# Kernel optimization log

Measured on AMD Instinct MI355X. Metric: run time of the kernel, lower is better.

The kernel has to match this reference:

```python
import jax, jax.numpy as jnp
import numpy as np

N_NODES = 100000
N_EDGES = 1200000
NODE_IN = 64
EDGE_IN = 32
HIDDEN = 64


def _glorot(key, shape):
    fan_in, fan_out = shape[0], shape[1]
    s = jnp.sqrt(2.0 / (fan_in + fan_out))
    return jax.random.normal(key, shape, dtype=jnp.float32) * s


def setup_inputs() -> dict:
    key = jax.random.key(0)
    ks = jax.random.split(key, 16)
    inp = {
        "x": jax.random.normal(ks[0], (N_NODES, NODE_IN), dtype=jnp.float32),
        "edge_index": jax.random.randint(ks[1], (2, N_EDGES), 0, N_NODES, dtype=jnp.int64),
        "edge_attr": jax.random.normal(ks[2], (N_EDGES, EDGE_IN), dtype=jnp.float32),
        # SAGE layer 0 (in=NODE_IN -> HIDDEN): lin_l (neighbors, has bias), lin_r (root)
        "w_l0": _glorot(ks[3], (NODE_IN, HIDDEN)),
        "w_r0": _glorot(ks[4], (NODE_IN, HIDDEN)),
        "b0": jnp.zeros((HIDDEN,), jnp.float32),
        "ln_g0": jnp.ones((HIDDEN,), jnp.float32),
        "ln_b0": jnp.zeros((HIDDEN,), jnp.float32),
        # SAGE layer 1 (HIDDEN -> HIDDEN)
        "w_l1": _glorot(ks[5], (HIDDEN, HIDDEN)),
        "w_r1": _glorot(ks[6], (HIDDEN, HIDDEN)),
        "b1": jnp.zeros((HIDDEN,), jnp.float32),
        "ln_g1": jnp.ones((HIDDEN,), jnp.float32),
        "ln_b1": jnp.zeros((HIDDEN,), jnp.float32),
        # Edge classifier MLP: in_dim = 3*HIDDEN + EDGE_IN = 224
        "cw1": _glorot(ks[7], (3 * HIDDEN + EDGE_IN, HIDDEN)),
        "cb1": jnp.zeros((HIDDEN,), jnp.float32),
        "cw2": _glorot(ks[8], (HIDDEN, HIDDEN // 2)),
        "cb2": jnp.zeros((HIDDEN // 2,), jnp.float32),
        "cw3": _glorot(ks[9], (HIDDEN // 2, 1)),
        "cb3": jnp.zeros((1,), jnp.float32),
    }
    return inp


def _sage_conv(x, src, dst, w_l, w_r, b):
    # mean-aggregate source features at destination nodes (PyG SAGEConv, aggr='mean')
    n = x.shape[0]
    msg = x[src]  # [E, F] gather
    agg = jax.ops.segment_sum(msg, dst, num_segments=n)
    cnt = jax.ops.segment_sum(jnp.ones((src.shape[0], 1), x.dtype), dst, num_segments=n)
    mean = agg / jnp.maximum(cnt, 1.0)
    return mean @ w_l + x @ w_r + b


def _layer_norm(x, g, b, eps=1e-5):
    mu = jnp.mean(x, axis=-1, keepdims=True)
    var = jnp.var(x, axis=-1, keepdims=True)
    return (x - mu) * jax.lax.rsqrt(var + eps) * g + b


def reference(x, edge_index, edge_attr,
              w_l0, w_r0, b0, ln_g0, ln_b0,
              w_l1, w_r1, b1, ln_g1, ln_b1,
              cw1, cb1, cw2, cb2, cw3, cb3):
    src, dst = edge_index[0], edge_index[1]
    # Encoder (eval mode: dropout is identity)
    h = jax.nn.relu(_layer_norm(_sage_conv(x, src, dst, w_l0, w_r0, b0), ln_g0, ln_b0))
    z = jax.nn.relu(_layer_norm(_sage_conv(h, src, dst, w_l1, w_r1, b1), ln_g1, ln_b1))
    # Edge classifier: gather-concat-MLP
    z_src = z[src]
    z_dst = z[dst]
    edge_repr = jnp.concatenate([z_src, z_dst, z_src * z_dst, edge_attr], axis=-1)
    h1 = jax.nn.relu(edge_repr @ cw1 + cb1)
    h2 = jax.nn.relu(h1 @ cw2 + cb2)
    logits = (h2 @ cw3 + cb3).squeeze(-1)  # [E]
    return logits
```

## Files before the change

kernel.cpp:

```cpp
#include <hip/hip_runtime.h>
#include <hip/hip_bf16.h>

#define N_NODES 100000
#define N_EDGES 1200000

typedef __attribute__((ext_vector_type(8))) short bfrag;
typedef __attribute__((ext_vector_type(4))) float ffrag;
typedef __attribute__((ext_vector_type(4))) float nf4;
typedef __attribute__((ext_vector_type(2))) float nf2;

union FragU { uint4 v; uint32_t u[4]; bfrag f; };

__device__ __forceinline__ ushort bfbits(float a) {
  union { __hip_bfloat16 h; ushort u; } c; c.h = __float2bfloat16(a); return c.u;
}
__device__ __forceinline__ uint32_t pkbf(float a, float b) {
  union { __hip_bfloat162 h; uint32_t u; } c;
  c.h = __float22bfloat162_rn(float2{a, b}); return c.u;
}
__device__ __forceinline__ uint32_t mul2bf(uint32_t a, uint32_t b) {
  union { uint32_t u; __hip_bfloat162 h; } x, y, r;
  x.u = a; y.u = b; r.h = __hmul2(x.h, y.h); return r.u;
}
__device__ __forceinline__ float bflo(uint32_t u) { return __int_as_float(u << 16); }
__device__ __forceinline__ float bfhi(uint32_t u) { return __int_as_float(u & 0xffff0000u); }

template <int CTRL>
__device__ __forceinline__ float dpp_add16(float v) {
  int x = __builtin_amdgcn_update_dpp(0, __float_as_int(v), CTRL, 0xF, 0xF, true);
  return v + __int_as_float(x);
}
__device__ __forceinline__ float reduce16(float v) {
  v = dpp_add16<0xB1>(v);
  v = dpp_add16<0x4E>(v);
  v = dpp_add16<0x141>(v);
  v = dpp_add16<0x140>(v);
  return v;
}


__global__ void cvt_k(const float* __restrict__ x, ushort* __restrict__ xb, int n2) {
  int i = blockIdx.x * blockDim.x + threadIdx.x;
  if (i < n2) {
    nf2 v = __builtin_nontemporal_load(((const nf2*)x) + i);
    ((uint32_t*)xb)[i] = pkbf(v.x, v.y);
  }
}


__global__ void hist_k(const int* __restrict__ ei, int* __restrict__ deg,
                       int* __restrict__ rank, int E) {
  int e = blockIdx.x * blockDim.x + threadIdx.x;
  if (e < E) rank[e] = atomicAdd(&deg[ei[E + e]], 1);
}

__global__ __launch_bounds__(1024) void scan1_k(const int* __restrict__ deg,
                                                int* __restrict__ off,
                                                int* __restrict__ bsum, int n) {
  __shared__ int wpart[16];
  __shared__ int wpre[16];
  int tid = threadIdx.x, lane = tid & 63, wid = tid >> 6;
  int i = blockIdx.x * 1024 + tid;
  int v = (i < n) ? deg[i] : 0;
  int x = v;
  #pragma unroll
  for (int o = 1; o < 64; o <<= 1) {
    int y = __shfl_up(x, o);
    if (lane >= o) x += y;
  }
  if (lane == 63) wpart[wid] = x;
  __syncthreads();
  if (tid == 0) {
    int run = 0;
    #pragma unroll
    for (int w = 0; w < 16; w++) { int t = wpart[w]; wpre[w] = run; run += t; }
    bsum[blockIdx.x] = run;
  }
  __syncthreads();
  if (i < n) off[i] = x - v + wpre[wid];
}

__global__ void scan2_k(const int* __restrict__ bsum, int* __restrict__ bpre,
                        int* __restrict__ off, int nb, int n) {
  if (threadIdx.x == 0) {
    int run = 0;
    for (int b = 0; b < nb; b++) { int t = bsum[b]; bpre[b] = run; run += t; }
    off[n] = run;
  }
}

__global__ __launch_bounds__(1024) void scan3_k(int* __restrict__ off,
                                                const int* __restrict__ bpre, int n) {
  int i = blockIdx.x * 1024 + threadIdx.x;
  if (i < n) off[i] += bpre[blockIdx.x];
}

__global__ void fill_k(const int* __restrict__ ei, const int* __restrict__ off,
                       const int* __restrict__ rank, int* __restrict__ csr, int E) {
  int e = blockIdx.x * blockDim.x + threadIdx.x;
  if (e < E) {
    int d = ei[E + e];
    int p = off[d] + rank[e];
    __builtin_nontemporal_store(ei[e], &csr[p]);
  }
}


__global__ __launch_bounds__(256) void agg_k(
    const ushort* __restrict__ Xb, const int* __restrict__ off, const int* __restrict__ csr,
    ushort* __restrict__ aggout, int n) {
  int lane = threadIdx.x & 63;
  int quad = lane >> 4, f8 = lane & 15;
  int wave = blockIdx.x * 4 + (threadIdx.x >> 6);
  int nw = gridDim.x * 4;
  int nquads = (n + 3) >> 2;
  const uint2* X2 = (const uint2*)Xb;
  for (int p = wave; p < nquads; p += nw) {
    int i = p * 4 + quad;
    int ic = i < n ? i : n - 1;
    int s0 = off[ic], s1 = off[ic + 1];
    float a0 = 0.f, a1 = 0.f, a2 = 0.f, a3 = 0.f;
    for (int j = s0; j < s1; j += 16) {
      int id[16]; uint2 us[16];
      #pragma unroll
      for (int u = 0; u < 16; u++) {
        int jj = j + u;
        id[u] = csr[jj < s1 ? jj : s1 - 1];
      }
      #pragma unroll
      for (int u = 0; u < 16; u++) us[u] = X2[(size_t)id[u] * 16 + f8];
      #pragma unroll
      for (int u = 0; u < 16; u++) {
        if (j + u < s1) {
          a0 += bflo(us[u].x); a1 += bfhi(us[u].x);
          a2 += bflo(us[u].y); a3 += bfhi(us[u].y);
        }
      }
    }
    if (i < n) {
      float rdeg = 1.f / fmaxf((float)(s1 - s0), 1.f);
      uint2 w;
      w.x = pkbf(a0 * rdeg, a1 * rdeg);
      w.y = pkbf(a2 * rdeg, a3 * rdeg);
      ((uint2*)aggout)[(size_t)i * 16 + f8] = w;
    }
  }
}


__global__ __launch_bounds__(256) void node_k(
    const ushort* __restrict__ agg, const ushort* __restrict__ selfb,
    const float* __restrict__ wl, const float* __restrict__ wr,
    const float* __restrict__ bias, const float* __restrict__ g, const float* __restrict__ lb,
    ushort* __restrict__ outb, int n) {
  __shared__ ushort wt[64 * 128];
  const int tid = threadIdx.x;
  for (int i = tid; i < 8192; i += 256) {
    int k = i >> 6, nn = i & 63;
    float v = (k < 64) ? wl[k * 64 + nn] : wr[(k - 64) * 64 + nn];
    wt[nn * 128 + (((k >> 3) ^ (nn & 7)) * 8) + (k & 7)] = bfbits(v);
  }
  __syncthreads();
  const int lane = tid & 63, wid = tid >> 6;
  const int ln = lane & 15, q = lane >> 4;
  float bias_n[4], g_n[4], lb_n[4];
  #pragma unroll
  for (int nt = 0; nt < 4; nt++) {
    bias_n[nt] = bias[nt * 16 + ln];
    g_n[nt] = g[nt * 16 + ln];
    lb_n[nt] = lb[nt * 16 + ln];
  }
  const int ntiles = (n + 15) >> 4;
  const int S = gridDim.x * 4;
  int t0 = blockIdx.x * 4 + wid;

  auto loadfrag = [&](FragU (&afr)[4], int t) {
    int tc = t < ntiles ? t : ntiles - 1;
    int node = tc * 16 + ln;
    int nc = node < n ? node : n - 1;
    #pragma unroll
    for (int kk = 0; kk < 2; kk++) {
      afr[kk].v     = ((const uint4*)agg)[(size_t)nc * 8 + kk * 4 + q];
      afr[2 + kk].v = ((const uint4*)selfb)[(size_t)nc * 8 + kk * 4 + q];
    }
  };

  auto compute = [&](FragU (&afr)[4], int t) {
    ffrag acc[4];
    #pragma unroll
    for (int nt = 0; nt < 4; nt++) acc[nt] = ffrag{0.f, 0.f, 0.f, 0.f};
    #pragma unroll
    for (int kk = 0; kk < 4; kk++) {
      bfrag a = afr[kk].f;
      #pragma unroll
      for (int nt = 0; nt < 4; nt++) {
        int nn = nt * 16 + ln;
        int b = kk * 4 + q;
        const bfrag* bp = (const bfrag*)&wt[nn * 128 + ((b ^ (nn & 7)) * 8)];
        acc[nt] = __builtin_amdgcn_mfma_f32_16x16x32_bf16(a, *bp, acc[nt], 0, 0, 0);
      }
    }
    #pragma unroll
    for (int r = 0; r < 4; r++) {
      int m = t * 16 + q * 4 + r;
      float o[4];
      #pragma unroll
      for (int nt = 0; nt < 4; nt++) o[nt] = acc[nt][r] + bias_n[nt];
      float s = (o[0] + o[1]) + (o[2] + o[3]);
      s = reduce16(s);
      float mu = s * (1.f / 64.f);
      float v2 = 0.f;
      #pragma unroll
      for (int nt = 0; nt < 4; nt++) { float d2 = o[nt] - mu; v2 += d2 * d2; }
      v2 = reduce16(v2);
      float rs = rsqrtf(v2 * (1.f / 64.f) + 1e-5f);
      if (m < n) {
        #pragma unroll
        for (int nt = 0; nt < 4; nt++) {
          float y = fmaxf((o[nt] - mu) * rs * g_n[nt] + lb_n[nt], 0.f);
          outb[(size_t)m * 64 + nt * 16 + ln] = bfbits(y);
        }
      }
    }
  };

  if (t0 >= ntiles) return;
  FragU fA[4], fB[4];
  loadfrag(fA, t0);
  loadfrag(fB, t0 + S);
  for (int t = t0; t < ntiles; t += 2 * S) {
    compute(fA, t);
    loadfrag(fA, t + 2 * S);
    if (t + S < ntiles) compute(fB, t + S);
    loadfrag(fB, t + 3 * S);
  }
}


__global__ __launch_bounds__(256, 2) void edge_mfma_k(
    const int* __restrict__ ei, const float* __restrict__ ea,
    const ushort* __restrict__ zb,
    const float* __restrict__ cw1, const float* __restrict__ cb1,
    const float* __restrict__ cw2, const float* __restrict__ cb2,
    const float* __restrict__ cw3, const float* __restrict__ cb3,
    float* __restrict__ out, int E) {
  __shared__ ushort smem[64 * 256];
  __shared__ ushort ws2[2048];
  const int tid = threadIdx.x;

  for (int i = tid; i < 224 * 64; i += 256) {
    int k = i >> 6, n = i & 63;
    int blk = k >> 3;
    smem[n * 256 + ((blk ^ (n & 7)) * 8) + (k & 7)] = bfbits(cw1[i]);
  }
  __syncthreads();

  const int lane = tid & 63, wid = tid >> 6;
  const int ln = lane & 15, q = lane >> 4;

  FragU w1f[7][4];
  #pragma unroll
  for (int kk = 0; kk < 7; kk++) {
    #pragma unroll
    for (int tt = 0; tt < 4; tt++) {
      int n = tt * 16 + ln;
      int b = kk * 4 + q;
      w1f[kk][tt].v = *(const uint4*)&smem[n * 256 + ((b ^ (n & 7)) * 8)];
    }
  }
  if (wid == 0) {
    #pragma unroll
    for (int t2 = 0; t2 < 2; t2++) {
      #pragma unroll
      for (int kk = 0; kk < 2; kk++) {
        uint32_t w[4];
        #pragma unroll
        for (int p = 0; p < 4; p++) {
          int k = kk * 32 + q * 8 + p * 2;
          int n = t2 * 16 + ln;
          w[p] = pkbf(cw2[k * 32 + n], cw2[(k + 1) * 32 + n]);
        }
        *(uint4*)&ws2[((t2 * 2 + kk) * 64 + lane) * 8] = make_uint4(w[0], w[1], w[2], w[3]);
      }
    }
  }
  __syncthreads();
  ushort* hb = &smem[wid * 1024];

  float cb1v[4];
  #pragma unroll
  for (int t = 0; t < 4; t++) cb1v[t] = cb1[t * 16 + ln];
  float cb2a = cb2[ln], cb2b = cb2[16 + ln];
  float w3a = cw3[ln], w3b = cw3[16 + ln];
  float cb3v = cb3[0];

  const int nt = E >> 4;
  const int S = gridDim.x * 4;
  const int S3 = 3 * S;
  const int w0 = blockIdx.x * 4 + wid;
  const uint4* Z4 = (const uint4*)zb;
  const nf4* EA4 = (const nf4*)ea;

  FragU zA[4], zB[4], zC[4];
  int svA, dvA, svB, dvB, svC, dvC;

  auto prol = [&](FragU (&z)[4], int &sv, int &dv, int u) {
    int uc = u < nt ? u : nt - 1;
    int e = uc * 16 + ln;
    int s = __builtin_nontemporal_load(ei + e);
    int d = __builtin_nontemporal_load(ei + E + e);
    z[0].v = Z4[(size_t)s * 8 + q];
    z[1].v = Z4[(size_t)s * 8 + 4 + q];
    z[2].v = Z4[(size_t)d * 8 + q];
    z[3].v = Z4[(size_t)d * 8 + 4 + q];
    int un = u + S3 < nt ? u + S3 : nt - 1;
    sv = __builtin_nontemporal_load(ei + un * 16 + ln);
    dv = __builtin_nontemporal_load(ei + E + un * 16 + ln);
  };
  prol(zA, svA, dvA, w0);
  prol(zB, svB, dvB, w0 + S);
  prol(zC, svC, dvC, w0 + 2 * S);

  auto half = [&](FragU (&z)[4], int &sv, int &dv, int u) {
    int uc = u < nt ? u : nt - 1;
    int e = uc * 16 + ln;
    nf4 l0 = __builtin_nontemporal_load(EA4 + (size_t)e * 8 + q * 2);
    nf4 l1 = __builtin_nontemporal_load(EA4 + (size_t)e * 8 + q * 2 + 1);

    ffrag acc1[4];
    #pragma unroll
    for (int tt = 0; tt < 4; tt++) acc1[tt] = ffrag{0.f, 0.f, 0.f, 0.f};
    #pragma unroll
    for (int kk = 0; kk < 7; kk++) {
      FragU af;
      if (kk < 4) af = z[kk];
      else if (kk < 6) {
        #pragma unroll
        for (int p = 0; p < 4; p++) af.u[p] = mul2bf(z[kk - 4].u[p], z[kk - 2].u[p]);
      } else {
        af.u[0] = pkbf(l0.x, l0.y); af.u[1] = pkbf(l0.z, l0.w);
        af.u[2] = pkbf(l1.x, l1.y); af.u[3] = pkbf(l1.z, l1.w);
      }
      bfrag a = af.f;
      #pragma unroll
      for (int tt = 0; tt < 4; tt++)
        acc1[tt] = __builtin_amdgcn_mfma_f32_16x16x32_bf16(a, w1f[kk][tt].f, acc1[tt], 0, 0, 0);
    }

    {
      z[0].v = Z4[(size_t)sv * 8 + q];
      z[1].v = Z4[(size_t)sv * 8 + 4 + q];
      z[2].v = Z4[(size_t)dv * 8 + q];
      z[3].v = Z4[(size_t)dv * 8 + 4 + q];
      int uf = u + 2 * S3 < nt ? u + 2 * S3 : nt - 1;
      sv = __builtin_nontemporal_load(ei + uf * 16 + ln);
      dv = __builtin_nontemporal_load(ei + E + uf * 16 + ln);
    }

    #pragma unroll
    for (int tt = 0; tt < 4; tt++) {
      #pragma unroll
      for (int r = 0; r < 4; r++) {
        int m = q * 4 + r;
        int col = tt * 16 + ln;
        float v = fmaxf(acc1[tt][r] + cb1v[tt], 0.f);
        hb[m * 64 + (((col >> 3) ^ (m & 7)) * 8) + (col & 7)] = bfbits(v);
      }
    }

    ffrag acc2[2];
    acc2[0] = ffrag{0.f, 0.f, 0.f, 0.f};
    acc2[1] = ffrag{0.f, 0.f, 0.f, 0.f};
    #pragma unroll
    for (int kk = 0; kk < 2; kk++) {
      int b = kk * 4 + q;
      const bfrag* ap = (const bfrag*)&hb[ln * 64 + ((b ^ (ln & 7)) * 8)];
      bfrag a2 = *ap;
      const bfrag* b0p = (const bfrag*)&ws2[((0 * 2 + kk) * 64 + lane) * 8];
      const bfrag* b1p = (const bfrag*)&ws2[((1 * 2 + kk) * 64 + lane) * 8];
      acc2[0] = __builtin_amdgcn_mfma_f32_16x16x32_bf16(a2, *b0p, acc2[0], 0, 0, 0);
      acc2[1] = __builtin_amdgcn_mfma_f32_16x16x32_bf16(a2, *b1p, acc2[1], 0, 0, 0);
    }

    float p0 = fmaxf(acc2[0][0] + cb2a, 0.f) * w3a + fmaxf(acc2[1][0] + cb2b, 0.f) * w3b;
    float p1 = fmaxf(acc2[0][1] + cb2a, 0.f) * w3a + fmaxf(acc2[1][1] + cb2b, 0.f) * w3b;
    float p2 = fmaxf(acc2[0][2] + cb2a, 0.f) * w3a + fmaxf(acc2[1][2] + cb2b, 0.f) * w3b;
    float p3 = fmaxf(acc2[0][3] + cb2a, 0.f) * w3a + fmaxf(acc2[1][3] + cb2b, 0.f) * w3b;
    p0 = reduce16(p0); p1 = reduce16(p1); p2 = reduce16(p2); p3 = reduce16(p3);
    float keep = (ln == 0) ? p0 : (ln == 1) ? p1 : (ln == 2) ? p2 : p3;
    if (u < nt && ln < 4)
      __builtin_nontemporal_store(keep + cb3v, &out[u * 16 + q * 4 + ln]);
  };

  for (int t = w0; t < nt; t += S3) {
    half(zA, svA, dvA, t);
    half(zB, svB, dvB, t + S);
    half(zC, svC, dvC, t + 2 * S);
  }
}


extern "C" void kernel_launch(void* const* d_in, const int* in_sizes, int n_in,
                              void* d_out, int out_size, void* d_ws, size_t ws_size,
                              hipStream_t stream) {
  const float* x   = (const float*)d_in[0];
  const int*   ei  = (const int*)d_in[1];
  const float* ea  = (const float*)d_in[2];
  const float* wl0 = (const float*)d_in[3];
  const float* wr0 = (const float*)d_in[4];
  const float* b0  = (const float*)d_in[5];
  const float* g0  = (const float*)d_in[6];
  const float* lb0 = (const float*)d_in[7];
  const float* wl1 = (const float*)d_in[8];
  const float* wr1 = (const float*)d_in[9];
  const float* b1  = (const float*)d_in[10];
  const float* g1  = (const float*)d_in[11];
  const float* lb1 = (const float*)d_in[12];
  const float* cw1 = (const float*)d_in[13];
  const float* cb1 = (const float*)d_in[14];
  const float* cw2 = (const float*)d_in[15];
  const float* cb2 = (const float*)d_in[16];
  const float* cw3 = (const float*)d_in[17];
  const float* cb3 = (const float*)d_in[18];
  float* out = (float*)d_out;
  const int N = N_NODES, E = N_EDGES;
  const int NB = (N + 1023) / 1024;

  uintptr_t pp = (uintptr_t)d_ws;
  auto alloc = [&](size_t bytes) {
    uintptr_t r = (pp + 255) & ~(uintptr_t)255; pp = r + bytes; return (void*)r;
  };
  int* deg  = (int*)alloc((size_t)N * 4);
  int* off  = (int*)alloc((size_t)(N + 1) * 4);
  int* rank = (int*)alloc((size_t)E * 4);
  int* csr  = (int*)alloc((size_t)E * 4);
  int* bsum = (int*)alloc((size_t)NB * 4);
  int* bpre = (int*)alloc((size_t)NB * 4);
  ushort* xb  = (ushort*)alloc((size_t)N * 64 * 2);
  ushort* agg = (ushort*)alloc((size_t)N * 64 * 2);
  ushort* hb  = (ushort*)alloc((size_t)N * 64 * 2);
  ushort* zb  = (ushort*)alloc((size_t)N * 64 * 2);

  hipMemsetAsync(deg, 0, (size_t)N * 4, stream);
  cvt_k<<<(N * 32 + 255) / 256, 256, 0, stream>>>(x, xb, N * 32);
  hist_k<<<(E + 255) / 256, 256, 0, stream>>>(ei, deg, rank, E);
  scan1_k<<<NB, 1024, 0, stream>>>(deg, off, bsum, N);
  scan2_k<<<1, 64, 0, stream>>>(bsum, bpre, off, NB, N);
  scan3_k<<<NB, 1024, 0, stream>>>(off, bpre, N);
  fill_k<<<(E + 255) / 256, 256, 0, stream>>>(ei, off, rank, csr, E);
  agg_k<<<2048, 256, 0, stream>>>(xb, off, csr, agg, N);
  node_k<<<1024, 256, 0, stream>>>(agg, xb, wl0, wr0, b0, g0, lb0, hb, N);
  agg_k<<<2048, 256, 0, stream>>>(hb, off, csr, agg, N);
  node_k<<<1024, 256, 0, stream>>>(agg, hb, wl1, wr1, b1, g1, lb1, zb, N);
  edge_mfma_k<<<512, 256, 0, stream>>>(ei, ea, zb, cw1, cb1, cw2, cb2, cw3, cb3, out, E);
}
```

Before: 503.4 us.

## Fuse neighbor aggregation into node MLP kernel and merge convert with histogram

```diff
diff --git a/kernel.cpp b/kernel.cpp
--- a/kernel.cpp
+++ b/kernel.cpp
@@ -39,20 +39,17 @@
 }
 
 
-__global__ void cvt_k(const float* __restrict__ x, ushort* __restrict__ xb, int n2) {
+__global__ void cvthist_k(const float* __restrict__ x, ushort* __restrict__ xb,
+                          const int* __restrict__ ei, int* __restrict__ deg,
+                          int* __restrict__ rank, int n2, int E) {
   int i = blockIdx.x * blockDim.x + threadIdx.x;
   if (i < n2) {
     nf2 v = __builtin_nontemporal_load(((const nf2*)x) + i);
     ((uint32_t*)xb)[i] = pkbf(v.x, v.y);
   }
-}
-
-
-__global__ void hist_k(const int* __restrict__ ei, int* __restrict__ deg,
-                       int* __restrict__ rank, int E) {
-  int e = blockIdx.x * blockDim.x + threadIdx.x;
-  if (e < E) rank[e] = atomicAdd(&deg[ei[E + e]], 1);
-}
+  if (i < E) rank[i] = atomicAdd(&deg[ei[E + i]], 1);
+}
+
 
 __global__ __launch_bounds__(1024) void scan1_k(const int* __restrict__ deg,
                                                 int* __restrict__ off,
@@ -101,59 +98,18 @@
   if (e < E) {
     int d = ei[E + e];
     int p = off[d] + rank[e];
-    __builtin_nontemporal_store(ei[e], &csr[p]);
-  }
-}
-
-
-__global__ __launch_bounds__(256) void agg_k(
+    csr[p] = ei[e];
+  }
+}
+
+
+__global__ __launch_bounds__(256) void layer_k(
     const ushort* __restrict__ Xb, const int* __restrict__ off, const int* __restrict__ csr,
-    ushort* __restrict__ aggout, int n) {
-  int lane = threadIdx.x & 63;
-  int quad = lane >> 4, f8 = lane & 15;
-  int wave = blockIdx.x * 4 + (threadIdx.x >> 6);
-  int nw = gridDim.x * 4;
-  int nquads = (n + 3) >> 2;
-  const uint2* X2 = (const uint2*)Xb;
-  for (int p = wave; p < nquads; p += nw) {
-    int i = p * 4 + quad;
-    int ic = i < n ? i : n - 1;
-    int s0 = off[ic], s1 = off[ic + 1];
-    float a0 = 0.f, a1 = 0.f, a2 = 0.f, a3 = 0.f;
-    for (int j = s0; j < s1; j += 16) {
-      int id[16]; uint2 us[16];
-      #pragma unroll
-      for (int u = 0; u < 16; u++) {
-        int jj = j + u;
-        id[u] = csr[jj < s1 ? jj : s1 - 1];
-      }
-      #pragma unroll
-      for (int u = 0; u < 16; u++) us[u] = X2[(size_t)id[u] * 16 + f8];
-      #pragma unroll
-      for (int u = 0; u < 16; u++) {
-        if (j + u < s1) {
-          a0 += bflo(us[u].x); a1 += bfhi(us[u].x);
-          a2 += bflo(us[u].y); a3 += bfhi(us[u].y);
-        }
-      }
-    }
-    if (i < n) {
-      float rdeg = 1.f / fmaxf((float)(s1 - s0), 1.f);
-      uint2 w;
-      w.x = pkbf(a0 * rdeg, a1 * rdeg);
-      w.y = pkbf(a2 * rdeg, a3 * rdeg);
-      ((uint2*)aggout)[(size_t)i * 16 + f8] = w;
-    }
-  }
-}
-
-
-__global__ __launch_bounds__(256) void node_k(
-    const ushort* __restrict__ agg, const ushort* __restrict__ selfb,
     const float* __restrict__ wl, const float* __restrict__ wr,
     const float* __restrict__ bias, const float* __restrict__ g, const float* __restrict__ lb,
     ushort* __restrict__ outb, int n) {
   __shared__ ushort wt[64 * 128];
+  __shared__ ushort mt[4][16 * 64];
   const int tid = threadIdx.x;
   for (int i = tid; i < 8192; i += 256) {
     int k = i >> 6, nn = i & 63;
@@ -170,22 +126,55 @@
     g_n[nt] = g[nt * 16 + ln];
     lb_n[nt] = lb[nt * 16 + ln];
   }
+  const uint2* X2 = (const uint2*)Xb;
+  ushort* mrow = mt[wid];
   const int ntiles = (n + 15) >> 4;
-  const int S = gridDim.x * 4;
-  int t0 = blockIdx.x * 4 + wid;
-
-  auto loadfrag = [&](FragU (&afr)[4], int t) {
-    int tc = t < ntiles ? t : ntiles - 1;
-    int node = tc * 16 + ln;
-    int nc = node < n ? node : n - 1;
+  for (int t = blockIdx.x * 4 + wid; t < ntiles; t += gridDim.x * 4) {
+    int node_s = t * 16 + ln;
+    int nc_s = node_s < n ? node_s : n - 1;
+    FragU sfr[2];
+    sfr[0].v = ((const uint4*)Xb)[(size_t)nc_s * 8 + q];
+    sfr[1].v = ((const uint4*)Xb)[(size_t)nc_s * 8 + 4 + q];
+
+    #pragma unroll
+    for (int r4 = 0; r4 < 4; r4++) {
+      int il = r4 * 4 + q;
+      int i = t * 16 + il;
+      int ic = i < n ? i : n - 1;
+      int s0 = off[ic], s1 = off[ic + 1];
+      float a0 = 0.f, a1 = 0.f, a2 = 0.f, a3 = 0.f;
+      for (int j = s0; j < s1; j += 16) {
+        int id[16]; uint2 us[16];
+        #pragma unroll
+        for (int u = 0; u < 16; u++) {
+          int jj = j + u;
+          id[u] = csr[jj < s1 ? jj : s1 - 1];
+        }
+        #pragma unroll
+        for (int u = 0; u < 16; u++) us[u] = X2[(size_t)id[u] * 16 + ln];
+        #pragma unroll
+        for (int u = 0; u < 16; u++) {
+          if (j + u < s1) {
+            a0 += bflo(us[u].x); a1 += bfhi(us[u].x);
+            a2 += bflo(us[u].y); a3 += bfhi(us[u].y);
+          }
+        }
+      }
+      float rdeg = 1.f / fmaxf((float)(s1 - s0), 1.f);
+      int c = (ln >> 1) ^ (il & 7);
+      uint2 w;
+      w.x = pkbf(a0 * rdeg, a1 * rdeg);
+      w.y = pkbf(a2 * rdeg, a3 * rdeg);
+      *(uint2*)&mrow[il * 64 + c * 8 + (ln & 1) * 4] = w;
+    }
+
+    FragU afr[4];
     #pragma unroll
     for (int kk = 0; kk < 2; kk++) {
-      afr[kk].v     = ((const uint4*)agg)[(size_t)nc * 8 + kk * 4 + q];
-      afr[2 + kk].v = ((const uint4*)selfb)[(size_t)nc * 8 + kk * 4 + q];
-    }
-  };
-
-  auto compute = [&](FragU (&afr)[4], int t) {
+      int c = kk * 4 + q;
+      afr[kk].v = *(const uint4*)&mrow[ln * 64 + ((c ^ (ln & 7)) * 8)];
+      afr[2 + kk] = sfr[kk];
+    }
     ffrag acc[4];
     #pragma unroll
     for (int nt = 0; nt < 4; nt++) acc[nt] = ffrag{0.f, 0.f, 0.f, 0.f};
@@ -222,17 +211,6 @@
         }
       }
     }
-  };
-
-  if (t0 >= ntiles) return;
-  FragU fA[4], fB[4];
-  loadfrag(fA, t0);
-  loadfrag(fB, t0 + S);
-  for (int t = t0; t < ntiles; t += 2 * S) {
-    compute(fA, t);
-    loadfrag(fA, t + 2 * S);
-    if (t + S < ntiles) compute(fB, t + S);
-    loadfrag(fB, t + 3 * S);
   }
 }
 
@@ -437,20 +415,18 @@
   int* bsum = (int*)alloc((size_t)NB * 4);
   int* bpre = (int*)alloc((size_t)NB * 4);
   ushort* xb  = (ushort*)alloc((size_t)N * 64 * 2);
-  ushort* agg = (ushort*)alloc((size_t)N * 64 * 2);
   ushort* hb  = (ushort*)alloc((size_t)N * 64 * 2);
   ushort* zb  = (ushort*)alloc((size_t)N * 64 * 2);
 
+  const int LGRID = (((N + 15) >> 4) + 3) / 4;
+
   hipMemsetAsync(deg, 0, (size_t)N * 4, stream);
-  cvt_k<<<(N * 32 + 255) / 256, 256, 0, stream>>>(x, xb, N * 32);
-  hist_k<<<(E + 255) / 256, 256, 0, stream>>>(ei, deg, rank, E);
+  cvthist_k<<<(N * 32 + 255) / 256, 256, 0, stream>>>(x, xb, ei, deg, rank, N * 32, E);
   scan1_k<<<NB, 1024, 0, stream>>>(deg, off, bsum, N);
   scan2_k<<<1, 64, 0, stream>>>(bsum, bpre, off, NB, N);
   scan3_k<<<NB, 1024, 0, stream>>>(off, bpre, N);
   fill_k<<<(E + 255) / 256, 256, 0, stream>>>(ei, off, rank, csr, E);
-  agg_k<<<2048, 256, 0, stream>>>(xb, off, csr, agg, N);
-  node_k<<<1024, 256, 0, stream>>>(agg, xb, wl0, wr0, b0, g0, lb0, hb, N);
-  agg_k<<<2048, 256, 0, stream>>>(hb, off, csr, agg, N);
-  node_k<<<1024, 256, 0, stream>>>(agg, hb, wl1, wr1, b1, g1, lb1, zb, N);
+  layer_k<<<LGRID, 256, 0, stream>>>(xb, off, csr, wl0, wr0, b0, g0, lb0, hb, N);
+  layer_k<<<LGRID, 256, 0, stream>>>(hb, off, csr, wl1, wr1, b1, g1, lb1, zb, N);
   edge_mfma_k<<<512, 256, 0, stream>>>(ei, ea, zb, cw1, cb1, cw2, cb2, cw3, cb3, out, E);
 }
```

Result: slower. 526.8 us (+4.6%).
